# Optimization experiments

Measured on AMD Instinct MI355X. Metric: run time of the kernel, lower is better.

## Reference

```python
import jax, jax.numpy as jnp
import numpy as np

EPS = 1e-7  # K.epsilon()
ATTN_WIDTH = 12
B, L, D = 8, 4096, 768


def setup_inputs() -> dict:
    key = jax.random.key(0)
    k1, k2 = jax.random.split(key)
    x = jax.random.normal(k1, (B, L, D), dtype=jnp.float32)
    Wa = jax.random.normal(k2, (D, 1), dtype=jnp.float32) * 0.05  # RandomNormal(stddev=0.05)
    return {"x": x, "Wa": Wa}


def reference(x, Wa):
    """Banded rank-1 self-attention.

    e[b,i,j] = u[b,i]*u[b,j] with u = x @ Wa, masked to the trailing band
    i-w+1 <= j <= i, normalized by the row sum (+eps), then v = a @ x.
    Because e is rank-1 inside the band, we never materialize the LxL matrix:
      wsum_i  = sum_{j=i-w+1}^{i} u_j          (windowed cumsum)
      wvec_i  = sum_{j=i-w+1}^{i} u_j * x_j    (windowed cumsum of u*x)
      v_i     = u_i * wvec_i / (u_i * wsum_i + eps)
    which is exactly e/(sum(e)+eps) @ x.
    """
    w = ATTN_WIDTH
    u = jnp.einsum('bld,do->bl', x, Wa)            # [B, L]
    cu = jnp.cumsum(u, axis=1)                      # [B, L]
    cux = jnp.cumsum(u[..., None] * x, axis=1)      # [B, L, D]
    # shifted[i] = cu[i-w] (0 for i < w)
    cu_shift = jnp.pad(cu, ((0, 0), (w, 0)))[:, :L]
    cux_shift = jnp.pad(cux, ((0, 0), (w, 0), (0, 0)))[:, :L, :]
    wsum = cu - cu_shift                            # [B, L]
    wvec = cux - cux_shift                          # [B, L, D]
    denom = u * wsum + EPS                          # [B, L]
    v = (u[..., None] * wvec) / denom[..., None]    # [B, L, D]
    return v
```

## Files before the change

kernel.cpp:

```cpp
#include <hip/hip_runtime.h>

typedef float vfloat4 __attribute__((ext_vector_type(4)));

namespace {
constexpr int kB = 8;
constexpr int kL = 4096;
constexpr int kD = 768;
constexpr int kW = 12;
constexpr int kHalo = kW - 1;
constexpr float kEps = 1e-7f;

constexpr int kT = 16;
constexpr int kRows = kT + kHalo;
constexpr int kThreads = 192;
constexpr int kChunks = kL / kT;
constexpr int kGrid = kB * kChunks;
constexpr int kGroups = kThreads / 4;
}

__global__ __launch_bounds__(kThreads, 3) void fused_onepass_kernel(
    const float* __restrict__ x, const float* __restrict__ Wa,
    float* __restrict__ out) {
  __shared__ double s_part[kRows][kGroups + 1];
  __shared__ double s_ud[kRows];
  __shared__ float s_scale[kT];

  const int blk = blockIdx.x;
  const int b = blk / kChunks;
  const int i0 = (blk % kChunks) * kT;
  const float* xb = x + (size_t)b * kL * kD;
  float* ob = out + (size_t)b * kL * kD;
  const int tid = threadIdx.x;
  const int c0 = 4 * tid;

  const vfloat4 w4 = *(const vfloat4*)(Wa + c0);

  vfloat4 xr[kRows];
  if (i0 >= kHalo) {
#pragma unroll
    for (int r = 0; r < kRows; ++r)
      xr[r] = *(const vfloat4*)(xb + (size_t)(i0 - kHalo + r) * kD + c0);
  } else {
#pragma unroll
    for (int r = 0; r < kRows; ++r) {
      const int row = i0 - kHalo + r;
      vfloat4 v = {0.f, 0.f, 0.f, 0.f};
      if (row >= 0) v = *(const vfloat4*)(xb + (size_t)row * kD + c0);
      xr[r] = v;
    }
  }

#pragma unroll
  for (int r = 0; r < kRows; ++r) {
    double p = (double)xr[r].x * (double)w4.x + (double)xr[r].y * (double)w4.y +
               (double)xr[r].z * (double)w4.z + (double)xr[r].w * (double)w4.w;
    p += __shfl_xor(p, 1, 64);
    p += __shfl_xor(p, 2, 64);
    if ((tid & 3) == 0) s_part[r][tid >> 2] = p;
  }
  __syncthreads();

  if (tid < kRows) {
    double a0 = 0.0, a1 = 0.0, a2 = 0.0, a3 = 0.0;
#pragma unroll
    for (int g = 0; g < kGroups; g += 4) {
      a0 += s_part[tid][g + 0];
      a1 += s_part[tid][g + 1];
      a2 += s_part[tid][g + 2];
      a3 += s_part[tid][g + 3];
    }
    s_ud[tid] = (a0 + a1) + (a2 + a3);
  }
  __syncthreads();

  if (tid < kT) {
    double wsum = 0.0;
#pragma unroll
    for (int k = 0; k < kW; ++k) wsum += s_ud[tid + k];
    const double uu = s_ud[tid + kHalo];
    s_scale[tid] = (float)(uu / (uu * wsum + (double)kEps));
  }

  float uf[kRows];
#pragma unroll
  for (int r = 0; r < kRows; ++r) uf[r] = (float)s_ud[r];
  __syncthreads();

#pragma unroll
  for (int t = 0; t < kT; ++t) {
    vfloat4 acc = {0.f, 0.f, 0.f, 0.f};
#pragma unroll
    for (int j = 0; j < kW; ++j) {
      const int r = kHalo + t - j;
      const float uu = uf[r];
      const vfloat4 xv = xr[r];
      acc.x += uu * xv.x; acc.y += uu * xv.y;
      acc.z += uu * xv.z; acc.w += uu * xv.w;
    }
    const float s = s_scale[t];
    vfloat4 o = {s * acc.x, s * acc.y, s * acc.z, s * acc.w};
    __builtin_nontemporal_store(o, (vfloat4*)(ob + (size_t)(i0 + t) * kD + c0));
  }
}

extern "C" void kernel_launch(void* const* d_in, const int* in_sizes, int n_in,
                              void* d_out, int out_size, void* d_ws, size_t ws_size,
                              hipStream_t stream) {
  const float* x = (const float*)d_in[0];
  const float* Wa = (const float*)d_in[1];
  float* out = (float*)d_out;
  (void)d_ws; (void)ws_size;

  fused_onepass_kernel<<<kGrid, kThreads, 0, stream>>>(x, Wa, out);
}
```

Before: 184.4 us.

## Process two chunks per block with register ring buffer to reuse halo rows

Each block now handles a 32-row strip in two 16-row chunks, keeping x rows in a register ring so the 11-row halo is loaded once per strip instead of once per chunk. Next-chunk rows are loaded during the output store loop, and their projections are reduced with a shuffle-based two-stage reduction. This trades fewer blocks and extra block-level synchronisation for less redundant global reads.

```diff
diff --git a/kernel.cpp b/kernel.cpp
--- a/kernel.cpp
+++ b/kernel.cpp
@@ -11,39 +11,47 @@
 constexpr float kEps = 1e-7f;
 
 constexpr int kT = 16;
-constexpr int kRows = kT + kHalo;
+constexpr int kC = 2;
+constexpr int kS = kT * kC;
+constexpr int kRing = kT + kHalo;
 constexpr int kThreads = 192;
-constexpr int kChunks = kL / kT;
-constexpr int kGrid = kB * kChunks;
+constexpr int kStrips = kL / kS;
+constexpr int kGrid = kB * kStrips;
 constexpr int kGroups = kThreads / 4;
+constexpr int kUMask = 31;
 }
 
-__global__ __launch_bounds__(kThreads, 3) void fused_onepass_kernel(
+__device__ __forceinline__ double dot4d(const vfloat4 a, const vfloat4 w) {
+  return (double)a.x * (double)w.x + (double)a.y * (double)w.y +
+         (double)a.z * (double)w.z + (double)a.w * (double)w.w;
+}
+
+__global__ __launch_bounds__(kThreads, 3) void banded_strip_kernel(
     const float* __restrict__ x, const float* __restrict__ Wa,
     float* __restrict__ out) {
-  __shared__ double s_part[kRows][kGroups + 1];
-  __shared__ double s_ud[kRows];
+  __shared__ double s_part[kRing][kGroups + 1];
+  __shared__ double s_ud[kUMask + 1];
+  __shared__ float s_uf[kUMask + 1];
   __shared__ float s_scale[kT];
 
   const int blk = blockIdx.x;
-  const int b = blk / kChunks;
-  const int i0 = (blk % kChunks) * kT;
+  const int b = blk / kStrips;
+  const int s0 = (blk % kStrips) * kS;
   const float* xb = x + (size_t)b * kL * kD;
   float* ob = out + (size_t)b * kL * kD;
   const int tid = threadIdx.x;
   const int c0 = 4 * tid;
-
   const vfloat4 w4 = *(const vfloat4*)(Wa + c0);
 
-  vfloat4 xr[kRows];
-  if (i0 >= kHalo) {
+  vfloat4 xr[kRing];
+  if (s0 >= kHalo) {
 #pragma unroll
-    for (int r = 0; r < kRows; ++r)
-      xr[r] = *(const vfloat4*)(xb + (size_t)(i0 - kHalo + r) * kD + c0);
+    for (int r = 0; r < kRing; ++r)
+      xr[r] = *(const vfloat4*)(xb + (size_t)(s0 - kHalo + r) * kD + c0);
   } else {
 #pragma unroll
-    for (int r = 0; r < kRows; ++r) {
-      const int row = i0 - kHalo + r;
+    for (int r = 0; r < kRing; ++r) {
+      const int row = s0 - kHalo + r;
       vfloat4 v = {0.f, 0.f, 0.f, 0.f};
       if (row >= 0) v = *(const vfloat4*)(xb + (size_t)row * kD + c0);
       xr[r] = v;
@@ -51,55 +59,81 @@
   }
 
 #pragma unroll
-  for (int r = 0; r < kRows; ++r) {
-    double p = (double)xr[r].x * (double)w4.x + (double)xr[r].y * (double)w4.y +
-               (double)xr[r].z * (double)w4.z + (double)xr[r].w * (double)w4.w;
+  for (int r = 0; r < kRing; ++r) {
+    double p = dot4d(xr[r], w4);
     p += __shfl_xor(p, 1, 64);
     p += __shfl_xor(p, 2, 64);
     if ((tid & 3) == 0) s_part[r][tid >> 2] = p;
   }
   __syncthreads();
-
-  if (tid < kRows) {
-    double a0 = 0.0, a1 = 0.0, a2 = 0.0, a3 = 0.0;
+  if (tid < 4 * kRing) {
+    const int r = tid >> 2, q = tid & 3;
+    double a = 0.0;
 #pragma unroll
-    for (int g = 0; g < kGroups; g += 4) {
-      a0 += s_part[tid][g + 0];
-      a1 += s_part[tid][g + 1];
-      a2 += s_part[tid][g + 2];
-      a3 += s_part[tid][g + 3];
-    }
-    s_ud[tid] = (a0 + a1) + (a2 + a3);
+    for (int g = 0; g < 12; ++g) a += s_part[r][q * 12 + g];
+    a += __shfl_xor(a, 1, 64);
+    a += __shfl_xor(a, 2, 64);
+    if (q == 0) { s_ud[r] = a; s_uf[r] = (float)a; }
   }
   __syncthreads();
 
-  if (tid < kT) {
-    double wsum = 0.0;
 #pragma unroll
-    for (int k = 0; k < kW; ++k) wsum += s_ud[tid + k];
-    const double uu = s_ud[tid + kHalo];
-    s_scale[tid] = (float)(uu / (uu * wsum + (double)kEps));
-  }
-
-  float uf[kRows];
+  for (int c = 0; c < kC; ++c) {
+    if (tid < kT) {
+      double wsum = 0.0;
 #pragma unroll
-  for (int r = 0; r < kRows; ++r) uf[r] = (float)s_ud[r];
-  __syncthreads();
+      for (int k = 0; k < kW; ++k) wsum += s_ud[(16 * c + tid + k) & kUMask];
+      const double uu = s_ud[(16 * c + tid + kHalo) & kUMask];
+      s_scale[tid] = (float)(uu / (uu * wsum + (double)kEps));
+    }
+    __syncthreads();
 
 #pragma unroll
-  for (int t = 0; t < kT; ++t) {
-    vfloat4 acc = {0.f, 0.f, 0.f, 0.f};
+    for (int t = 0; t < kT; ++t) {
+      vfloat4 acc = {0.f, 0.f, 0.f, 0.f};
 #pragma unroll
-    for (int j = 0; j < kW; ++j) {
-      const int r = kHalo + t - j;
-      const float uu = uf[r];
-      const vfloat4 xv = xr[r];
-      acc.x += uu * xv.x; acc.y += uu * xv.y;
-      acc.z += uu * xv.z; acc.w += uu * xv.w;
+      for (int j = 0; j < kW; ++j) {
+        const int l = 16 * c + t + kHalo - j;
+        const float uu = s_uf[l & kUMask];
+        const vfloat4 xv = xr[l % kRing];
+        acc.x += uu * xv.x; acc.y += uu * xv.y;
+        acc.z += uu * xv.z; acc.w += uu * xv.w;
+      }
+      const float s = s_scale[t];
+      vfloat4 o = {s * acc.x, s * acc.y, s * acc.z, s * acc.w};
+      __builtin_nontemporal_store(o, (vfloat4*)(ob + (size_t)(s0 + 16 * c + t) * kD + c0));
+      if (c + 1 < kC) {
+        const int lnew = kRing + 16 * c + t;
+        xr[lnew % kRing] =
+            *(const vfloat4*)(xb + (size_t)(s0 - kHalo + lnew) * kD + c0);
+      }
     }
-    const float s = s_scale[t];
-    vfloat4 o = {s * acc.x, s * acc.y, s * acc.z, s * acc.w};
-    __builtin_nontemporal_store(o, (vfloat4*)(ob + (size_t)(i0 + t) * kD + c0));
+
+    if (c + 1 < kC) {
+#pragma unroll
+      for (int t = 0; t < kT; ++t) {
+        const int lnew = kRing + 16 * c + t;
+        double p = dot4d(xr[lnew % kRing], w4);
+        p += __shfl_xor(p, 1, 64);
+        p += __shfl_xor(p, 2, 64);
+        if ((tid & 3) == 0) s_part[t][tid >> 2] = p;
+      }
+      __syncthreads();
+      if (tid < 64) {
+        const int r = tid >> 2, q = tid & 3;
+        double a = 0.0;
+#pragma unroll
+        for (int g = 0; g < 12; ++g) a += s_part[r][q * 12 + g];
+        a += __shfl_xor(a, 1, 64);
+        a += __shfl_xor(a, 2, 64);
+        if (q == 0) {
+          const int l = kRing + 16 * c + r;
+          s_ud[l & kUMask] = a;
+          s_uf[l & kUMask] = (float)a;
+        }
+      }
+      __syncthreads();
+    }
   }
 }
 
@@ -111,5 +145,5 @@
   float* out = (float*)d_out;
   (void)d_ws; (void)ws_size;
 
-  fused_onepass_kernel<<<kGrid, kThreads, 0, stream>>>(x, Wa, out);
+  banded_strip_kernel<<<kGrid, kThreads, 0, stream>>>(x, Wa, out);
 }
```

After: 184.3 us. Within noise of the previous version (-0.0%).
